# Kernel tuning notes

Hardware: AMD Instinct MI355X
Metric: run time of the kernel (lower is better)

The kernel has to match this reference:

```python
import jax, jax.numpy as jnp
import numpy as np
from functools import partial

FEAT = 12544  # 64 * 14 * 14, CfC input_size
UNITS = 64
BB = 128      # ncps CfC default backbone_units (backbone_layers=1)
N_ACTIONS = 8


def lecun_tanh(x):
    return 1.7159 * jnp.tanh(0.666 * x)


def setup_inputs() -> dict:
    key = jax.random.key(0)
    ks = jax.random.split(key, 20)
    s = 0.05
    inp = {
        "x": jax.random.normal(ks[0], (16, 64, 3, 62, 62), dtype=jnp.float32),
        "conv1_w": jax.random.normal(ks[1], (32, 3, 4, 4), dtype=jnp.float32) * s,
        "conv1_b": jnp.zeros((32,), dtype=jnp.float32),
        "conv2_w": jax.random.normal(ks[2], (64, 32, 4, 4), dtype=jnp.float32) * s,
        "conv2_b": jnp.zeros((64,), dtype=jnp.float32),
        "W_bb": jax.random.normal(ks[3], (FEAT + UNITS, BB), dtype=jnp.float32) * 0.01,
        "b_bb": jnp.zeros((BB,), dtype=jnp.float32),
        "W_ff1": jax.random.normal(ks[4], (BB, UNITS), dtype=jnp.float32) * s,
        "b_ff1": jnp.zeros((UNITS,), dtype=jnp.float32),
        "W_ff2": jax.random.normal(ks[5], (BB, UNITS), dtype=jnp.float32) * s,
        "b_ff2": jnp.zeros((UNITS,), dtype=jnp.float32),
        "W_ta": jax.random.normal(ks[6], (BB, UNITS), dtype=jnp.float32) * s,
        "b_ta": jnp.zeros((UNITS,), dtype=jnp.float32),
        "W_tb": jax.random.normal(ks[7], (BB, UNITS), dtype=jnp.float32) * s,
        "b_tb": jnp.zeros((UNITS,), dtype=jnp.float32),
        "W_out": jax.random.normal(ks[8], (UNITS, N_ACTIONS), dtype=jnp.float32) * s,
        "b_out": jnp.zeros((N_ACTIONS,), dtype=jnp.float32),
    }
    return inp


def _conv(x, w, b):
    y = jax.lax.conv_general_dilated(
        x, w, window_strides=(2, 2), padding="VALID",
        dimension_numbers=("NCHW", "OIHW", "NCHW"))
    return jax.nn.relu(y + b[None, :, None, None])


def reference(x, conv1_w, conv1_b, conv2_w, conv2_b, W_bb, b_bb,
              W_ff1, b_ff1, W_ff2, b_ff2, W_ta, b_ta, W_tb, b_tb,
              W_out, b_out):
    B, T, C, H, W = x.shape
    c_in = x.reshape(B * T, C, H, W)
    h = _conv(c_in, conv1_w, conv1_b)          # [BT,32,30,30]
    h = _conv(h, conv2_w, conv2_b)             # [BT,64,14,14]
    feat = h.reshape(B, T, FEAT)               # torch Flatten order == NCHW reshape

    # CfC (ncps, mode='default', backbone_layers=1, ts=1.0), return_sequences=False
    W_in, W_h = W_bb[:FEAT], W_bb[FEAT:]
    # precompute input contribution to backbone for all timesteps
    u = jnp.einsum("btf,fk->btk", feat, W_in) + b_bb   # [B,T,BB]

    def step(hid, u_t):
        z = lecun_tanh(u_t + hid @ W_h)                # backbone activation
        ff1 = jnp.tanh(z @ W_ff1 + b_ff1)
        ff2 = jnp.tanh(z @ W_ff2 + b_ff2)
        t_interp = jax.nn.sigmoid((z @ W_ta + b_ta) + (z @ W_tb + b_tb))  # ts=1.0
        hid_new = ff1 * (1.0 - t_interp) + t_interp * ff2
        return hid_new, None

    h0 = jnp.zeros((B, UNITS), dtype=x.dtype)
    h_last, _ = jax.lax.scan(step, h0, jnp.swapaxes(u, 0, 1))  # scan over time
    return h_last @ W_out + b_out
```

## Files before the change

### kernel.cpp

```cpp
#include <hip/hip_runtime.h>
#include <hip/hip_bf16.h>
#include <math.h>

#define FEATN 12544
#define NIMG 1024
#define PLANEP 482

typedef __attribute__((ext_vector_type(8))) short short8;
typedef __attribute__((ext_vector_type(4))) float f32x4;

#define OFF_W1F   0
#define OFF_W2F   6144
#define OFF_WBBF  71680
#define OFF_FEATB 62265344
#define OFF_U     87955456
#define OFF_PART  88479744
#define OFF_WHF   103163904
#define OFF_WGF   103180288
#define WS_BYTES  103245824

__device__ __forceinline__ unsigned short f2bf(float v) {
    union { float f; unsigned int u; } c; c.f = v;
    unsigned int r = c.u + 0x7FFFu + ((c.u >> 16) & 1u);
    return (unsigned short)(r >> 16);
}
__device__ __forceinline__ unsigned int pack2bf(float lo, float hi) {
    return (unsigned int)f2bf(lo) | ((unsigned int)f2bf(hi) << 16);
}

__device__ __forceinline__ float lecun_tanh_fast(float x) {
    float e = __builtin_amdgcn_exp2f(1.9216698f * x);
    return 1.7159f - 3.4318f * __builtin_amdgcn_rcpf(e + 1.f);
}
__device__ __forceinline__ float tanh_fast(float x) {
    float e = __builtin_amdgcn_exp2f(2.8853901f * x);
    return 1.f - 2.f * __builtin_amdgcn_rcpf(e + 1.f);
}
__device__ __forceinline__ float sigmoid_fast(float x) {
    float e = __builtin_amdgcn_exp2f(-1.4426950f * x);
    return __builtin_amdgcn_rcpf(1.f + e);
}

__global__ __launch_bounds__(256) void prep_all(const float* __restrict__ w1, const float* __restrict__ w2,
                         const float* __restrict__ Wbb,
                         const float* __restrict__ Wff1, const float* __restrict__ Wff2,
                         const float* __restrict__ Wta,  const float* __restrict__ Wtb,
                         unsigned short* __restrict__ w1f, unsigned short* __restrict__ w2f,
                         unsigned short* __restrict__ wbbf,
                         unsigned short* __restrict__ whf, unsigned short* __restrict__ wgf) {
    int bid = blockIdx.x, tid = threadIdx.x;
    if (bid < 6272) {
        int i = bid * 256 + tid;
        int j = i & 7, lane = (i >> 3) & 63, nt = (i >> 9) & 7, kstep = i >> 12;
        int f = kstep * 32 + (lane >> 4) * 8 + j;
        int col = nt * 16 + (lane & 15);
        wbbf[i] = f2bf(Wbb[(size_t)f * 128 + col]);
    } else if (bid < 6400) {
        int i = (bid - 6272) * 256 + tid;
        int j = i & 7, lane = (i >> 3) & 63, kstep = (i >> 9) & 15, nt = i >> 13;
        int oc = nt * 16 + (lane & 15);
        int ic = 2 * kstep + (j >> 2);
        int ky = lane >> 4, kx = j & 3;
        w2f[i] = f2bf(w2[oc * 512 + ic * 16 + ky * 4 + kx]);
    } else if (bid < 6528) {
        int i = (bid - 6400) * 256 + tid;
        int j = i & 7, lane = (i >> 3) & 63, nt = (i >> 9) & 15, kstep = (i >> 13) & 3;
        int k = kstep * 32 + ((lane >> 4) & 3) * 8 + j;
        int m = nt >> 2;
        int c = (nt & 3) * 16 + (lane & 15);
        float v;
        if (m == 0)      v = Wff1[k * 64 + c];
        else if (m == 1) v = Wff2[k * 64 + c];
        else if (m == 2) v = Wta[k * 64 + c] + Wtb[k * 64 + c];
        else             v = 0.f;
        wgf[i] = f2bf(v);
    } else if (bid < 6560) {
        int i = (bid - 6528) * 256 + tid;
        int j = i & 7, lane = (i >> 3) & 63, nt = (i >> 9) & 7, kstep = (i >> 12) & 1;
        int k = kstep * 32 + ((lane >> 4) & 3) * 8 + j;
        int col = nt * 16 + (lane & 15);
        whf[i] = f2bf(Wbb[(size_t)(FEATN + k) * 128 + col]);
    } else {
        int i = (bid - 6560) * 256 + tid;
        if (i >= 2048) return;
        int j = i & 7, lane = (i >> 3) & 63, nt = (i >> 9) & 1, kstep = (i >> 10) & 1;
        int oc = nt * 16 + (lane & 15);
        int ky = (lane >> 4) & 3, kx = j & 3;
        float v;
        if (kstep == 0) { int ic = j >> 2; v = w1[oc * 48 + ic * 16 + ky * 4 + kx]; }
        else            { v = (j >> 2) == 0 ? w1[oc * 48 + 32 + ky * 4 + kx] : 0.f; }
        w1f[i] = f2bf(v);
    }
}

__global__ __launch_bounds__(512) void fused_conv(const float* __restrict__ x,
                                                  const float* __restrict__ b1,
                                                  const unsigned short* __restrict__ w1f,
                                                  const float* __restrict__ b2,
                                                  const unsigned short* __restrict__ w2f,
                                                  unsigned short* __restrict__ featb) {
    __shared__ unsigned short h1s[32 * 2 * PLANEP];
    int img = blockIdx.x;
    int tid = threadIdx.x;
    int lane = tid & 63, wid = tid >> 6;
    int rowl = lane & 15, g = lane >> 4;
    const float* xg = x + (size_t)img * 11532;

    {
        short8 bfr[2][2];
        #pragma unroll
        for (int ks = 0; ks < 2; ++ks)
            #pragma unroll
            for (int nt = 0; nt < 2; ++nt)
                bfr[ks][nt] = *(const short8*)(w1f + (((ks * 2 + nt) * 64 + lane) << 3));
        float bias0 = b1[rowl], bias1 = b1[16 + rowl];

        #pragma unroll
        for (int i = 0; i < 8; ++i) {
            int mtile = wid + 8 * i;
            if (mtile >= 57) break;
            int m = mtile * 16 + rowl; if (m > 899) m = 899;
            int oy = m / 30, ox = m - oy * 30;
            int y = 2 * oy + g, x0 = 2 * ox;
            const float* xb = xg + y * 62 + x0;
            union { unsigned int u[4]; short8 s; } af0, af1;
            #pragma unroll
            for (int c = 0; c < 2; ++c) {
                float2 p0 = *(const float2*)(xb + c * 3844);
                float2 p1 = *(const float2*)(xb + c * 3844 + 2);
                af0.u[c * 2]     = pack2bf(p0.x, p0.y);
                af0.u[c * 2 + 1] = pack2bf(p1.x, p1.y);
            }
            {
                float2 q0 = *(const float2*)(xb + 7688);
                float2 q1 = *(const float2*)(xb + 7690);
                af1.u[0] = pack2bf(q0.x, q0.y);
                af1.u[1] = pack2bf(q1.x, q1.y);
                af1.u[2] = 0; af1.u[3] = 0;
            }
            f32x4 acc0 = (f32x4){0.f, 0.f, 0.f, 0.f};
            f32x4 acc1 = (f32x4){0.f, 0.f, 0.f, 0.f};
            acc0 = __builtin_amdgcn_mfma_f32_16x16x32_bf16(af0.s, bfr[0][0], acc0, 0, 0, 0);
            acc0 = __builtin_amdgcn_mfma_f32_16x16x32_bf16(af1.s, bfr[1][0], acc0, 0, 0, 0);
            acc1 = __builtin_amdgcn_mfma_f32_16x16x32_bf16(af0.s, bfr[0][1], acc1, 0, 0, 0);
            acc1 = __builtin_amdgcn_mfma_f32_16x16x32_bf16(af1.s, bfr[1][1], acc1, 0, 0, 0);
            int sp0 = mtile * 16 + g * 4;
            int oy0 = sp0 / 30, ox0 = sp0 - oy0 * 30;
            #pragma unroll
            for (int nt = 0; nt < 2; ++nt) {
                f32x4 a = nt ? acc1 : acc0;
                int oc = nt * 16 + rowl;
                float bias = nt ? bias1 : bias0;
                int pbase = oc * (2 * PLANEP);
                #pragma unroll
                for (int r = 0; r < 4; ++r) {
                    if (sp0 + r > 899) break;
                    int oxr = ox0 + r, oyr = oy0;
                    if (oxr >= 30) { oxr -= 30; ++oyr; }
                    h1s[pbase + oyr * 32 + oxr] = f2bf(fmaxf(a[r] + bias, 0.f));
                }
            }
        }
    }
    __syncthreads();

    f32x4 acc[2][4];
    #pragma unroll
    for (int i = 0; i < 2; ++i)
        #pragma unroll
        for (int nt = 0; nt < 4; ++nt) acc[i][nt] = (f32x4){0.f, 0.f, 0.f, 0.f};

    int dofs[2];
    #pragma unroll
    for (int i = 0; i < 2; ++i) {
        int mtile = wid + 8 * i;
        int m = mtile * 16 + rowl; if (m > 195) m = 195;
        int oy = m / 14, ox = m - oy * 14;
        int y = 2 * oy + g, x0 = 2 * ox;
        dofs[i] = y * 16 + (x0 >> 1);
    }
    const unsigned int* lds32 = (const unsigned int*)h1s;

    #pragma unroll 4
    for (int kstep = 0; kstep < 16; ++kstep) {
        short8 bfr[4];
        #pragma unroll
        for (int nt = 0; nt < 4; ++nt)
            bfr[nt] = *(const short8*)(w2f + (((nt * 16 + kstep) * 64 + lane) << 3));
        int icb = kstep * 2 * PLANEP;
        #pragma unroll
        for (int i = 0; i < 2; ++i) {
            int mtile = wid + 8 * i;
            if (mtile < 13) {
                int dof = icb + dofs[i];
                union { unsigned int u[4]; short8 s; } af;
                af.u[0] = lds32[dof];
                af.u[1] = lds32[dof + 1];
                af.u[2] = lds32[dof + PLANEP];
                af.u[3] = lds32[dof + PLANEP + 1];
                #pragma unroll
                for (int nt = 0; nt < 4; ++nt)
                    acc[i][nt] = __builtin_amdgcn_mfma_f32_16x16x32_bf16(af.s, bfr[nt], acc[i][nt], 0, 0, 0);
            }
        }
    }
    #pragma unroll
    for (int i = 0; i < 2; ++i) {
        int mtile = wid + 8 * i;
        if (mtile >= 13) continue;
        int sp0 = mtile * 16 + g * 4;
        #pragma unroll
        for (int nt = 0; nt < 4; ++nt) {
            int oc = nt * 16 + rowl;
            float bias = b2[oc];
            unsigned short pk[4];
            #pragma unroll
            for (int r = 0; r < 4; ++r)
                pk[r] = f2bf(fmaxf(acc[i][nt][r] + bias, 0.f));
            unsigned short* dstp = featb + (size_t)img * 12544 + oc * 196 + sp0;
            if (sp0 + 3 < 196) {
                *(uint2*)dstp = *(uint2*)pk;
            } else {
                #pragma unroll
                for (int r = 0; r < 4; ++r) if (sp0 + r < 196) dstp[r] = pk[r];
            }
        }
    }
}

__global__ __launch_bounds__(256) void gemm_u_mfma(const unsigned short* __restrict__ featb,
                                                   const unsigned short* __restrict__ Wbbf,
                                                   float* __restrict__ part) {
    int tid = threadIdx.x, lane = tid & 63, wid = tid >> 6;
    int rowl = lane & 15, g = lane >> 4;
    int m0 = blockIdx.x * 64 + wid * 16;
    int ks0 = blockIdx.y * 14;
    f32x4 acc[8];
    #pragma unroll
    for (int nt = 0; nt < 8; ++nt) acc[nt] = (f32x4){0.f, 0.f, 0.f, 0.f};
    const unsigned short* arow = featb + (size_t)(m0 + rowl) * FEATN + g * 8;
    #pragma unroll 2
    for (int kk = 0; kk < 14; ++kk) {
        int kstep = ks0 + kk;
        short8 afr = *(const short8*)(arow + kstep * 32);
        #pragma unroll
        for (int nt = 0; nt < 8; ++nt) {
            short8 bfr = *(const short8*)(Wbbf + ((((size_t)kstep * 8 + nt) * 64 + lane) << 3));
            acc[nt] = __builtin_amdgcn_mfma_f32_16x16x32_bf16(afr, bfr, acc[nt], 0, 0, 0);
        }
    }
    float* pg = part + (size_t)blockIdx.y * 131072;
    #pragma unroll
    for (int nt = 0; nt < 8; ++nt)
        #pragma unroll
        for (int r = 0; r < 4; ++r)
            pg[(m0 + g * 4 + r) * 128 + nt * 16 + rowl] = acc[nt][r];
}

__global__ void reduce_u(const float4* __restrict__ part4, const float* __restrict__ bbb,
                         float4* __restrict__ u4) {
    int o = blockIdx.x * 256 + threadIdx.x;
    int c4 = o & 31, b = (o >> 5) & 15, t = o >> 9;
    int m = b * 64 + t;
    float4 s = *(const float4*)(bbb + c4 * 4);
    #pragma unroll
    for (int ks = 0; ks < 28; ++ks) {
        float4 p = part4[(size_t)ks * 32768 + m * 32 + c4];
        s.x += p.x; s.y += p.y; s.z += p.z; s.w += p.w;
    }
    u4[(size_t)t * 512 + b * 32 + c4] = s;
}

__global__ __launch_bounds__(256, 1) void rnn_mfma(const float* __restrict__ u,
                                                   const unsigned short* __restrict__ whf,
                                                   const unsigned short* __restrict__ wgf,
                                                   const float* __restrict__ bff1,
                                                   const float* __restrict__ bff2,
                                                   const float* __restrict__ bta,
                                                   const float* __restrict__ btb,
                                                   const float* __restrict__ Wout,
                                                   const float* __restrict__ bout,
                                                   float* __restrict__ out) {
    __shared__ unsigned short hidA[16 * 64];
    __shared__ unsigned short zA[16 * 128];
    int tid = threadIdx.x, lane = tid & 63, w = tid >> 6;
    int rowl = lane & 15, g = lane >> 4;

    for (int idx = tid; idx < 1024; idx += 256) hidA[idx] = 0;

    short8 wh_r[2][2];
    #pragma unroll
    for (int ks = 0; ks < 2; ++ks)
        #pragma unroll
        for (int ntl = 0; ntl < 2; ++ntl)
            wh_r[ks][ntl] = *(const short8*)(whf + (((ks * 8 + 2 * w + ntl) * 64 + lane) << 3));
    short8 wg_r[3][4];
    #pragma unroll
    for (int m = 0; m < 3; ++m)
        #pragma unroll
        for (int ks = 0; ks < 4; ++ks)
            wg_r[m][ks] = *(const short8*)(wgf + (((ks * 16 + 4 * m + w) * 64 + lane) << 3));

    int cc = w * 16 + rowl;
    float bias1 = bff1[cc], bias2 = bff2[cc], biast = bta[cc] + btb[cc];

    float upf[8];
    #pragma unroll
    for (int i = 0; i < 8; ++i) {
        int ntl = i >> 2, r = i & 3;
        upf[i] = u[(g * 4 + r) * 128 + (2 * w + ntl) * 16 + rowl];
    }
    __syncthreads();

    float hidv[4];
    #pragma unroll 1
    for (int t = 0; t < 64; ++t) {
        short8 ah[2];
        #pragma unroll
        for (int ks = 0; ks < 2; ++ks) {
            int byte = (rowl * 128 + ks * 64 + g * 16) ^ ((rowl & 7) << 4);
            ah[ks] = *(const short8*)((const char*)hidA + byte);
        }
        f32x4 zacc[2];
        #pragma unroll
        for (int ntl = 0; ntl < 2; ++ntl) {
            zacc[ntl] = (f32x4){upf[ntl * 4 + 0], upf[ntl * 4 + 1], upf[ntl * 4 + 2], upf[ntl * 4 + 3]};
            #pragma unroll
            for (int ks = 0; ks < 2; ++ks)
                zacc[ntl] = __builtin_amdgcn_mfma_f32_16x16x32_bf16(ah[ks], wh_r[ks][ntl], zacc[ntl], 0, 0, 0);
        }
        if (t < 63) {
            #pragma unroll
            for (int i = 0; i < 8; ++i) {
                int ntl = i >> 2, r = i & 3;
                upf[i] = u[(t + 1) * 2048 + (g * 4 + r) * 128 + (2 * w + ntl) * 16 + rowl];
            }
        }
        #pragma unroll
        for (int ntl = 0; ntl < 2; ++ntl)
            #pragma unroll
            for (int r = 0; r < 4; ++r) {
                float zv = lecun_tanh_fast(zacc[ntl][r]);
                int row = g * 4 + r, c = w * 32 + ntl * 16 + rowl;
                int byte = (row * 256 + c * 2) ^ ((row & 7) << 4);
                *(unsigned short*)((char*)zA + byte) = f2bf(zv);
            }
        __syncthreads();
        short8 zfr[4];
        #pragma unroll
        for (int ks = 0; ks < 4; ++ks) {
            int byte = (rowl * 256 + ks * 64 + g * 16) ^ ((rowl & 7) << 4);
            zfr[ks] = *(const short8*)((const char*)zA + byte);
        }
        f32x4 facc[3];
        facc[0] = (f32x4){bias1, bias1, bias1, bias1};
        facc[1] = (f32x4){bias2, bias2, bias2, bias2};
        facc[2] = (f32x4){biast, biast, biast, biast};
        #pragma unroll
        for (int m = 0; m < 3; ++m)
            #pragma unroll
            for (int ks = 0; ks < 4; ++ks)
                facc[m] = __builtin_amdgcn_mfma_f32_16x16x32_bf16(zfr[ks], wg_r[m][ks], facc[m], 0, 0, 0);
        #pragma unroll
        for (int r = 0; r < 4; ++r) {
            float ff1 = tanh_fast(facc[0][r]);
            float ff2 = tanh_fast(facc[1][r]);
            float tt  = sigmoid_fast(facc[2][r]);
            float hv  = ff1 + tt * (ff2 - ff1);
            hidv[r] = hv;
            int row = g * 4 + r;
            int byte = (row * 128 + cc * 2) ^ ((row & 7) << 4);
            *(unsigned short*)((char*)hidA + byte) = f2bf(hv);
        }
        __syncthreads();
    }

    float* hf = (float*)zA;
    #pragma unroll
    for (int r = 0; r < 4; ++r) hf[(g * 4 + r) * 64 + cc] = hidv[r];
    __syncthreads();
    if (tid < 128) {
        int b = tid >> 3, a = tid & 7;
        float s = bout[a];
        #pragma unroll
        for (int j = 0; j < 64; ++j) s += hf[b * 64 + j] * Wout[j * 8 + a];
        out[tid] = s;
    }
}

extern "C" void kernel_launch(void* const* d_in, const int* in_sizes, int n_in,
                              void* d_out, int out_size, void* d_ws, size_t ws_size,
                              hipStream_t stream) {
    const float* x    = (const float*)d_in[0];
    const float* w1   = (const float*)d_in[1];
    const float* b1   = (const float*)d_in[2];
    const float* w2   = (const float*)d_in[3];
    const float* b2   = (const float*)d_in[4];
    const float* Wbb  = (const float*)d_in[5];
    const float* bbb  = (const float*)d_in[6];
    const float* Wff1 = (const float*)d_in[7];
    const float* bff1 = (const float*)d_in[8];
    const float* Wff2 = (const float*)d_in[9];
    const float* bff2 = (const float*)d_in[10];
    const float* Wta  = (const float*)d_in[11];
    const float* bta  = (const float*)d_in[12];
    const float* Wtb  = (const float*)d_in[13];
    const float* btb  = (const float*)d_in[14];
    const float* Wout = (const float*)d_in[15];
    const float* bout = (const float*)d_in[16];

    if (ws_size < (size_t)WS_BYTES) return;

    char* wsb = (char*)d_ws;
    unsigned short* w1f   = (unsigned short*)(wsb + OFF_W1F);
    unsigned short* w2f   = (unsigned short*)(wsb + OFF_W2F);
    unsigned short* wbbf  = (unsigned short*)(wsb + OFF_WBBF);
    unsigned short* featb = (unsigned short*)(wsb + OFF_FEATB);
    float*          u     = (float*)(wsb + OFF_U);
    float*          part  = (float*)(wsb + OFF_PART);
    unsigned short* whf   = (unsigned short*)(wsb + OFF_WHF);
    unsigned short* wgf   = (unsigned short*)(wsb + OFF_WGF);

    prep_all<<<6568, 256, 0, stream>>>(w1, w2, Wbb, Wff1, Wff2, Wta, Wtb,
                                       w1f, w2f, wbbf, whf, wgf);
    fused_conv<<<1024, 512, 0, stream>>>(x, b1, w1f, b2, w2f, featb);
    gemm_u_mfma<<<dim3(16, 28), 256, 0, stream>>>(featb, wbbf, part);
    reduce_u<<<128, 256, 0, stream>>>((const float4*)part, bbb, (float4*)u);
    rnn_mfma<<<1, 256, 0, stream>>>(u, whf, wgf, bff1, bff2, bta, btb, Wout, bout, (float*)d_out);
}
```

Baseline: 120.9 us.

## Use cheaper bf16 rounding, transpose u for vector loads, pack z stores

Replaces round-to-nearest-even bf16 conversion with a cheaper round-half-up in the conv and RNN paths. The reduce kernel now writes u in a transposed layout, so the serial RNN kernel can prefetch each timestep with two float4 loads instead of eight scalar loads. The z activations are written to LDS as packed pairs of bf16, with the gate weight K ordering permuted to match. The single-block RNN loop is latency-bound, so fewer loads and stores per step target the critical path, at the cost of strided scalar stores in reduce_u and slightly different rounding.

Result: faster. 115.3 us (median of 3 runs) (-4.7%).

```diff
diff --git a/kernel.cpp b/kernel.cpp
--- a/kernel.cpp
+++ b/kernel.cpp
@@ -24,8 +24,13 @@
     unsigned int r = c.u + 0x7FFFu + ((c.u >> 16) & 1u);
     return (unsigned short)(r >> 16);
 }
-__device__ __forceinline__ unsigned int pack2bf(float lo, float hi) {
-    return (unsigned int)f2bf(lo) | ((unsigned int)f2bf(hi) << 16);
+__device__ __forceinline__ unsigned short f2bf_rhu(float v) {
+    union { float f; unsigned int u; } c; c.f = v;
+    return (unsigned short)((c.u + 0x8000u) >> 16);
+}
+__device__ __forceinline__ unsigned int pack2bf_rhu(float lo, float hi) {
+    union { float f; unsigned int u; } a, b; a.f = lo; b.f = hi;
+    return ((a.u + 0x8000u) >> 16) | ((b.u + 0x8000u) & 0xFFFF0000u);
 }
 
 __device__ __forceinline__ float lecun_tanh_fast(float x) {
@@ -65,7 +70,8 @@
     } else if (bid < 6528) {
         int i = (bid - 6400) * 256 + tid;
         int j = i & 7, lane = (i >> 3) & 63, nt = (i >> 9) & 15, kstep = (i >> 13) & 3;
-        int k = kstep * 32 + ((lane >> 4) & 3) * 8 + j;
+        int gq = (lane >> 4) & 3;
+        int k = kstep * 32 + (j & 1) * 16 + gq * 4 + (j >> 1);
         int m = nt >> 2;
         int c = (nt & 3) * 16 + (lane & 15);
         float v;
@@ -128,14 +134,14 @@
             for (int c = 0; c < 2; ++c) {
                 float2 p0 = *(const float2*)(xb + c * 3844);
                 float2 p1 = *(const float2*)(xb + c * 3844 + 2);
-                af0.u[c * 2]     = pack2bf(p0.x, p0.y);
-                af0.u[c * 2 + 1] = pack2bf(p1.x, p1.y);
+                af0.u[c * 2]     = pack2bf_rhu(p0.x, p0.y);
+                af0.u[c * 2 + 1] = pack2bf_rhu(p1.x, p1.y);
             }
             {
                 float2 q0 = *(const float2*)(xb + 7688);
                 float2 q1 = *(const float2*)(xb + 7690);
-                af1.u[0] = pack2bf(q0.x, q0.y);
-                af1.u[1] = pack2bf(q1.x, q1.y);
+                af1.u[0] = pack2bf_rhu(q0.x, q0.y);
+                af1.u[1] = pack2bf_rhu(q1.x, q1.y);
                 af1.u[2] = 0; af1.u[3] = 0;
             }
             f32x4 acc0 = (f32x4){0.f, 0.f, 0.f, 0.f};
@@ -157,7 +163,7 @@
                     if (sp0 + r > 899) break;
                     int oxr = ox0 + r, oyr = oy0;
                     if (oxr >= 30) { oxr -= 30; ++oyr; }
-                    h1s[pbase + oyr * 32 + oxr] = f2bf(fmaxf(a[r] + bias, 0.f));
+                    h1s[pbase + oyr * 32 + oxr] = f2bf_rhu(fmaxf(a[r] + bias, 0.f));
                 }
             }
         }
@@ -216,7 +222,7 @@
             unsigned short pk[4];
             #pragma unroll
             for (int r = 0; r < 4; ++r)
-                pk[r] = f2bf(fmaxf(acc[i][nt][r] + bias, 0.f));
+                pk[r] = f2bf_rhu(fmaxf(acc[i][nt][r] + bias, 0.f));
             unsigned short* dstp = featb + (size_t)img * 12544 + oc * 196 + sp0;
             if (sp0 + 3 < 196) {
                 *(uint2*)dstp = *(uint2*)pk;
@@ -258,7 +264,7 @@
 }
 
 __global__ void reduce_u(const float4* __restrict__ part4, const float* __restrict__ bbb,
-                         float4* __restrict__ u4) {
+                         float* __restrict__ u) {
     int o = blockIdx.x * 256 + threadIdx.x;
     int c4 = o & 31, b = (o >> 5) & 15, t = o >> 9;
     int m = b * 64 + t;
@@ -268,7 +274,11 @@
         float4 p = part4[(size_t)ks * 32768 + m * 32 + c4];
         s.x += p.x; s.y += p.y; s.z += p.z; s.w += p.w;
     }
-    u4[(size_t)t * 512 + b * 32 + c4] = s;
+    int cb = c4 * 4;
+    u[((size_t)t * 128 + cb + 0) * 16 + b] = s.x;
+    u[((size_t)t * 128 + cb + 1) * 16 + b] = s.y;
+    u[((size_t)t * 128 + cb + 2) * 16 + b] = s.z;
+    u[((size_t)t * 128 + cb + 3) * 16 + b] = s.w;
 }
 
 __global__ __launch_bounds__(256, 1) void rnn_mfma(const float* __restrict__ u,
@@ -304,11 +314,14 @@
     int cc = w * 16 + rowl;
     float bias1 = bff1[cc], bias2 = bff2[cc], biast = bta[cc] + btb[cc];
 
-    float upf[8];
-    #pragma unroll
-    for (int i = 0; i < 8; ++i) {
-        int ntl = i >> 2, r = i & 3;
-        upf[i] = u[(g * 4 + r) * 128 + (2 * w + ntl) * 16 + rowl];
+    const float* ub0 = u + ((size_t)(2 * w) * 16 + rowl) * 16 + g * 4;
+    const float* ub1 = u + ((size_t)(2 * w + 1) * 16 + rowl) * 16 + g * 4;
+    f32x4 upf[2];
+    {
+        float4 v0 = *(const float4*)ub0;
+        float4 v1 = *(const float4*)ub1;
+        upf[0] = (f32x4){v0.x, v0.y, v0.z, v0.w};
+        upf[1] = (f32x4){v1.x, v1.y, v1.z, v1.w};
     }
     __syncthreads();
 
@@ -324,27 +337,25 @@
         f32x4 zacc[2];
         #pragma unroll
         for (int ntl = 0; ntl < 2; ++ntl) {
-            zacc[ntl] = (f32x4){upf[ntl * 4 + 0], upf[ntl * 4 + 1], upf[ntl * 4 + 2], upf[ntl * 4 + 3]};
+            zacc[ntl] = upf[ntl];
             #pragma unroll
             for (int ks = 0; ks < 2; ++ks)
                 zacc[ntl] = __builtin_amdgcn_mfma_f32_16x16x32_bf16(ah[ks], wh_r[ks][ntl], zacc[ntl], 0, 0, 0);
         }
         if (t < 63) {
-            #pragma unroll
-            for (int i = 0; i < 8; ++i) {
-                int ntl = i >> 2, r = i & 3;
-                upf[i] = u[(t + 1) * 2048 + (g * 4 + r) * 128 + (2 * w + ntl) * 16 + rowl];
-            }
-        }
-        #pragma unroll
-        for (int ntl = 0; ntl < 2; ++ntl)
-            #pragma unroll
-            for (int r = 0; r < 4; ++r) {
-                float zv = lecun_tanh_fast(zacc[ntl][r]);
-                int row = g * 4 + r, c = w * 32 + ntl * 16 + rowl;
-                int byte = (row * 256 + c * 2) ^ ((row & 7) << 4);
-                *(unsigned short*)((char*)zA + byte) = f2bf(zv);
-            }
+            float4 v0 = *(const float4*)(ub0 + (size_t)(t + 1) * 2048);
+            float4 v1 = *(const float4*)(ub1 + (size_t)(t + 1) * 2048);
+            upf[0] = (f32x4){v0.x, v0.y, v0.z, v0.w};
+            upf[1] = (f32x4){v1.x, v1.y, v1.z, v1.w};
+        }
+        #pragma unroll
+        for (int r = 0; r < 4; ++r) {
+            float z0 = lecun_tanh_fast(zacc[0][r]);
+            float z1 = lecun_tanh_fast(zacc[1][r]);
+            int row = g * 4 + r;
+            int byte = (row * 256 + w * 64 + rowl * 4) ^ ((row & 7) << 4);
+            *(unsigned int*)((char*)zA + byte) = pack2bf_rhu(z0, z1);
+        }
         __syncthreads();
         short8 zfr[4];
         #pragma unroll
@@ -370,7 +381,7 @@
             hidv[r] = hv;
             int row = g * 4 + r;
             int byte = (row * 128 + cc * 2) ^ ((row & 7) << 4);
-            *(unsigned short*)((char*)hidA + byte) = f2bf(hv);
+            *(unsigned short*)((char*)hidA + byte) = f2bf_rhu(hv);
         }
         __syncthreads();
     }
@@ -425,6 +436,6 @@
                                        w1f, w2f, wbbf, whf, wgf);
     fused_conv<<<1024, 512, 0, stream>>>(x, b1, w1f, b2, w2f, featb);
     gemm_u_mfma<<<dim3(16, 28), 256, 0, stream>>>(featb, wbbf, part);
-    reduce_u<<<128, 256, 0, stream>>>((const float4*)part, bbb, (float4*)u);
+    reduce_u<<<128, 256, 0, stream>>>((const float4*)part, bbb, u);
     rnn_mfma<<<1, 256, 0, stream>>>(u, whf, wgf, bff1, bff2, bta, btb, Wout, bout, (float*)d_out);
 }
```
